# Kernel optimization log

Hardware: AMD Instinct MI355X
Metric: run time of the kernel (lower is better)

## Reference

```python
import jax, jax.numpy as jnp
import numpy as np

T = 2048        # tokens (flattened)
H = 2048        # hidden_size
NH = 16         # num_attention_heads
NKV = 4         # num_key_value_heads
HD = H // NH    # head_dim = 128
E = 8           # num_local_experts
TOPK = 2        # num_experts_per_tok
DFF = 4096      # expert intermediate size
EPS = 1e-5
THETA = 1000000.0


def setup_inputs() -> dict:
    key = jax.random.key(0)
    ks = jax.random.split(key, 10)
    s = 0.02
    return {
        "positions": jnp.arange(T, dtype=jnp.int32),
        "hidden_states": jax.random.normal(ks[0], (T, H), jnp.float32),
        "residual": jax.random.normal(ks[1], (T, H), jnp.float32),
        "ln1_w": jnp.ones((H,), jnp.float32),
        "ln2_w": jnp.ones((H,), jnp.float32),
        "wq": jax.random.normal(ks[2], (H, NH * HD), jnp.float32) * s,
        "wk": jax.random.normal(ks[3], (H, NKV * HD), jnp.float32) * s,
        "wv": jax.random.normal(ks[4], (H, NKV * HD), jnp.float32) * s,
        "wo": jax.random.normal(ks[5], (NH * HD, H), jnp.float32) * s,
        "gate_w": jax.random.normal(ks[6], (H, E), jnp.float32) * s,
        "w1": jax.random.normal(ks[7], (E, H, DFF), jnp.float32) * s,
        "w3": jax.random.normal(ks[8], (E, H, DFF), jnp.float32) * s,
        "w2": jax.random.normal(ks[9], (E, DFF, H), jnp.float32) * s,
    }


def _rmsnorm(x, w):
    v = jnp.mean(x * x, axis=-1, keepdims=True)
    return x * jax.lax.rsqrt(v + EPS) * w


def _rope(pos, x):
    # NeoX-style rotary; x: [T, nh, HD]
    half = HD // 2
    inv_freq = 1.0 / (THETA ** (jnp.arange(half, dtype=jnp.float32) / half))
    ang = pos.astype(jnp.float32)[:, None] * inv_freq          # [T, half]
    cos = jnp.cos(ang)[:, None, :]
    sin = jnp.sin(ang)[:, None, :]
    x1, x2 = jnp.split(x, 2, axis=-1)
    return jnp.concatenate([x1 * cos - x2 * sin, x2 * cos + x1 * sin], axis=-1)


def _forward(positions, hidden_states, residual, ln1_w, ln2_w,
             wq, wk, wv, wo, gate_w, w1, w3, w2):
    # fused add + RMSNorm (vLLM semantics)
    res = hidden_states + residual
    h = _rmsnorm(res, ln1_w)

    # attention with RoPE + GQA, causal
    q = (h @ wq).reshape(T, NH, HD)
    k = (h @ wk).reshape(T, NKV, HD)
    v = (h @ wv).reshape(T, NKV, HD)
    q = _rope(positions, q)
    k = _rope(positions, k)
    rep = NH // NKV
    k = jnp.repeat(k, rep, axis=1)   # [T, NH, HD]
    v = jnp.repeat(v, rep, axis=1)
    scores = jnp.einsum("thd,shd->hts", q, k) * (HD ** -0.5)   # [NH, T, T]
    causal = jnp.tril(jnp.ones((T, T), bool))
    scores = jnp.where(causal[None], scores, jnp.finfo(scores.dtype).min)
    p = jax.nn.softmax(scores, axis=-1)
    attn = jnp.einsum("hts,shd->thd", p, v).reshape(T, NH * HD) @ wo

    # fused add + RMSNorm
    res2 = attn + res
    h2 = _rmsnorm(res2, ln2_w)

    # MoE: softmax gate (fp32), top-k, renormalize, combine
    logits = h2 @ gate_w
    rw = jax.nn.softmax(logits.astype(jnp.float32), axis=-1)   # [T, E]
    w_top, idx = jax.lax.top_k(rw, TOPK)                        # [T, K]
    w_top = w_top / jnp.sum(w_top, axis=-1, keepdims=True)
    # per-token combine weight for each expert (sums duplicate selections)
    comb = jnp.zeros((T, E), jnp.float32).at[
        jnp.arange(T)[:, None], idx].add(w_top)                 # [T, E]

    out = jnp.zeros((T, H), h2.dtype)
    for e in range(E):  # small fixed expert count
        g = jax.nn.silu(h2 @ w1[e]) * (h2 @ w3[e])
        out = out + comb[:, e:e + 1] * (g @ w2[e])
    return out, res2


def reference(positions, hidden_states, residual, ln1_w, ln2_w,
              wq, wk, wv, wo, gate_w, w1, w3, w2):
    return _forward(positions, hidden_states, residual, ln1_w, ln2_w,
                    wq, wk, wv, wo, gate_w, w1, w3, w2)
```

## Files before the change

kernel.cpp:

```cpp
#include <hip/hip_runtime.h>
#include <math.h>

typedef unsigned short u16;
typedef __attribute__((ext_vector_type(8))) short bf16x8;
typedef __attribute__((ext_vector_type(4))) float f32x4;

#define DI __device__ __forceinline__

constexpr int Tt  = 2048;
constexpr int Hh  = 2048;
constexpr int DFFd = 4096;

DI u16 f2b(float f) {
  union { float f; unsigned u; } x; x.f = f;
  unsigned r = x.u + 0x7fffu + ((x.u >> 16) & 1u);
  return (u16)(r >> 16);
}
DI float b2f(u16 h) {
  union { unsigned u; float f; } x; x.u = ((unsigned)h) << 16; return x.f;
}
DI void gll16(const void* g, void* l) {
  __builtin_amdgcn_global_load_lds((const __attribute__((address_space(1))) unsigned int*)g,
                                   (__attribute__((address_space(3))) unsigned int*)l, 16, 0, 0);
}

__global__ void k_addnorm(const float* __restrict__ hs, const float* __restrict__ resid,
                          const float* __restrict__ w, float* __restrict__ resf,
                          u16* __restrict__ hb, u16* __restrict__ hblo) {
  const int t = blockIdx.x, tid = threadIdx.x, lane = tid & 63, wid = tid >> 6;
  __shared__ float red[4];
  const size_t base = (size_t)t * Hh;
  float4 a = *(const float4*)(hs + base + tid * 4);
  float4 b = *(const float4*)(resid + base + tid * 4);
  float4 c = *(const float4*)(hs + base + 1024 + tid * 4);
  float4 d = *(const float4*)(resid + base + 1024 + tid * 4);
  float4 r1 = {a.x + b.x, a.y + b.y, a.z + b.z, a.w + b.w};
  float4 r2 = {c.x + d.x, c.y + d.y, c.z + d.z, c.w + d.w};
  *(float4*)(resf + base + tid * 4) = r1;
  *(float4*)(resf + base + 1024 + tid * 4) = r2;
  float ss = r1.x*r1.x + r1.y*r1.y + r1.z*r1.z + r1.w*r1.w
           + r2.x*r2.x + r2.y*r2.y + r2.z*r2.z + r2.w*r2.w;
#pragma unroll
  for (int m = 1; m < 64; m <<= 1) ss += __shfl_xor(ss, m);
  if (lane == 0) red[wid] = ss;
  __syncthreads();
  float tot = red[0] + red[1] + red[2] + red[3];
  float rstd = rsqrtf(tot * (1.f / Hh) + 1e-5f);
  float4 w1v = *(const float4*)(w + tid * 4);
  float4 w2v = *(const float4*)(w + 1024 + tid * 4);
  float hv[8];
  hv[0] = r1.x * rstd * w1v.x; hv[1] = r1.y * rstd * w1v.y;
  hv[2] = r1.z * rstd * w1v.z; hv[3] = r1.w * rstd * w1v.w;
  hv[4] = r2.x * rstd * w2v.x; hv[5] = r2.y * rstd * w2v.y;
  hv[6] = r2.z * rstd * w2v.z; hv[7] = r2.w * rstd * w2v.w;
  ushort4 o1, o2, l1, l2;
  u16 h;
  h = f2b(hv[0]); o1.x = h; l1.x = f2b(hv[0] - b2f(h));
  h = f2b(hv[1]); o1.y = h; l1.y = f2b(hv[1] - b2f(h));
  h = f2b(hv[2]); o1.z = h; l1.z = f2b(hv[2] - b2f(h));
  h = f2b(hv[3]); o1.w = h; l1.w = f2b(hv[3] - b2f(h));
  h = f2b(hv[4]); o2.x = h; l2.x = f2b(hv[4] - b2f(h));
  h = f2b(hv[5]); o2.y = h; l2.y = f2b(hv[5] - b2f(h));
  h = f2b(hv[6]); o2.z = h; l2.z = f2b(hv[6] - b2f(h));
  h = f2b(hv[7]); o2.w = h; l2.w = f2b(hv[7] - b2f(h));
  *(ushort4*)(hb + base + tid * 4) = o1;
  *(ushort4*)(hb + base + 1024 + tid * 4) = o2;
  *(ushort4*)(hblo + base + tid * 4) = l1;
  *(ushort4*)(hblo + base + 1024 + tid * 4) = l2;
}

__global__ void k_transpose64(const float* __restrict__ src, u16* __restrict__ dst,
                              int K, int N) {
  size_t zo = (size_t)blockIdx.z * K * N;
  src += zo; dst += zo;
  __shared__ float tl[64][65];
  const int t = threadIdx.x;
  const int k0 = blockIdx.x * 64, n0 = blockIdx.y * 64;
  int r = t >> 4, c = (t & 15) * 4;
#pragma unroll
  for (int u = 0; u < 4; u++) {
    float4 v = *(const float4*)(src + (size_t)(k0 + r + u * 16) * N + n0 + c);
    tl[r + u * 16][c] = v.x; tl[r + u * 16][c + 1] = v.y;
    tl[r + u * 16][c + 2] = v.z; tl[r + u * 16][c + 3] = v.w;
  }
  __syncthreads();
  int n = t >> 2, kc = (t & 3) * 16;
  __align__(16) u16 tmp[16];
#pragma unroll
  for (int i = 0; i < 16; i++) tmp[i] = f2b(tl[kc + i][n]);
  uint4* dp = (uint4*)(dst + (size_t)(n0 + n) * K + k0 + kc);
  dp[0] = ((uint4*)tmp)[0];
  dp[1] = ((uint4*)tmp)[1];
}

__global__ void k_transpose2_64(const float* __restrict__ src, u16* __restrict__ dhi,
                                u16* __restrict__ dlo, int K, int N) {
  __shared__ float tl[64][65];
  const int t = threadIdx.x;
  const int k0 = blockIdx.x * 64, n0 = blockIdx.y * 64;
  int r = t >> 4, c = (t & 15) * 4;
#pragma unroll
  for (int u = 0; u < 4; u++) {
    float4 v = *(const float4*)(src + (size_t)(k0 + r + u * 16) * N + n0 + c);
    tl[r + u * 16][c] = v.x; tl[r + u * 16][c + 1] = v.y;
    tl[r + u * 16][c + 2] = v.z; tl[r + u * 16][c + 3] = v.w;
  }
  __syncthreads();
  int n = t >> 2, kc = (t & 3) * 16;
  __align__(16) u16 th[16], tlo[16];
#pragma unroll
  for (int i = 0; i < 16; i++) {
    float x = tl[kc + i][n];
    u16 hx = f2b(x);
    th[i] = hx; tlo[i] = f2b(x - b2f(hx));
  }
  uint4* dph = (uint4*)(dhi + (size_t)(n0 + n) * K + k0 + kc);
  dph[0] = ((uint4*)th)[0]; dph[1] = ((uint4*)th)[1];
  uint4* dpl = (uint4*)(dlo + (size_t)(n0 + n) * K + k0 + kc);
  dpl[0] = ((uint4*)tlo)[0]; dpl[1] = ((uint4*)tlo)[1];
}

__launch_bounds__(256, 2)
__global__ void gemm_qkv(const u16* __restrict__ Ahi, const u16* __restrict__ Alo,
                         const u16* __restrict__ Bhi, const u16* __restrict__ Blo,
                         float* __restrict__ C) {
  __shared__ __align__(16) u16 Ah[2][128 * 32];
  __shared__ __align__(16) u16 Al[2][128 * 32];
  __shared__ __align__(16) u16 Bh[2][128 * 32];
  __shared__ __align__(16) u16 Bl[2][128 * 32];
  const int tid = threadIdx.x;
  const int wid = tid >> 6, lane = tid & 63, lr = lane & 15, lg = lane >> 4;
  const int m0 = blockIdx.x * 128, n0 = blockIdx.y * 128;
  const int wm = (wid >> 1) * 64, wn = (wid & 1) * 64;
  const int c0 = tid, c1 = tid + 256;
  const int ss0 = ((c0 & 3) ^ ((c0 >> 3) & 3)) * 8;
  const int ss1 = ((c1 & 3) ^ ((c1 >> 3) & 3)) * 8;
  const int fs = (lg ^ ((lr >> 1) & 3)) * 8;
  const size_t ao0 = (size_t)(m0 + (c0 >> 2)) * 2048 + ss0;
  const size_t ao1 = (size_t)(m0 + (c1 >> 2)) * 2048 + ss1;
  const size_t bo0 = (size_t)(n0 + (c0 >> 2)) * 2048 + ss0;
  const size_t bo1 = (size_t)(n0 + (c1 >> 2)) * 2048 + ss1;
  f32x4 zv = {0.f, 0.f, 0.f, 0.f};
  f32x4 acc[4][4];
#pragma unroll
  for (int i = 0; i < 4; i++)
#pragma unroll
    for (int j = 0; j < 4; j++) acc[i][j] = zv;
  const int NT = 2048 >> 5;
  gll16(Ahi + ao0, &Ah[0][c0 * 8]); gll16(Ahi + ao1, &Ah[0][c1 * 8]);
  gll16(Alo + ao0, &Al[0][c0 * 8]); gll16(Alo + ao1, &Al[0][c1 * 8]);
  gll16(Bhi + bo0, &Bh[0][c0 * 8]); gll16(Bhi + bo1, &Bh[0][c1 * 8]);
  gll16(Blo + bo0, &Bl[0][c0 * 8]); gll16(Blo + bo1, &Bl[0][c1 * 8]);
  int cur = 0;
  for (int t = 0; t < NT; ++t) {
    __syncthreads();
    if (t + 1 < NT) {
      int ko = (t + 1) << 5;
      gll16(Ahi + ao0 + ko, &Ah[cur ^ 1][c0 * 8]); gll16(Ahi + ao1 + ko, &Ah[cur ^ 1][c1 * 8]);
      gll16(Alo + ao0 + ko, &Al[cur ^ 1][c0 * 8]); gll16(Alo + ao1 + ko, &Al[cur ^ 1][c1 * 8]);
      gll16(Bhi + bo0 + ko, &Bh[cur ^ 1][c0 * 8]); gll16(Bhi + bo1 + ko, &Bh[cur ^ 1][c1 * 8]);
      gll16(Blo + bo0 + ko, &Bl[cur ^ 1][c0 * 8]); gll16(Blo + bo1 + ko, &Bl[cur ^ 1][c1 * 8]);
    }
    bf16x8 ah[4], al[4], bh[4], bl[4];
#pragma unroll
    for (int i = 0; i < 4; i++) {
      ah[i] = *(const bf16x8*)&Ah[cur][(wm + i * 16 + lr) * 32 + fs];
      al[i] = *(const bf16x8*)&Al[cur][(wm + i * 16 + lr) * 32 + fs];
    }
#pragma unroll
    for (int j = 0; j < 4; j++) {
      bh[j] = *(const bf16x8*)&Bh[cur][(wn + j * 16 + lr) * 32 + fs];
      bl[j] = *(const bf16x8*)&Bl[cur][(wn + j * 16 + lr) * 32 + fs];
    }
#pragma unroll
    for (int i = 0; i < 4; i++)
#pragma unroll
      for (int j = 0; j < 4; j++) {
        acc[i][j] = __builtin_amdgcn_mfma_f32_16x16x32_bf16(ah[i], bh[j], acc[i][j], 0, 0, 0);
        acc[i][j] = __builtin_amdgcn_mfma_f32_16x16x32_bf16(ah[i], bl[j], acc[i][j], 0, 0, 0);
        acc[i][j] = __builtin_amdgcn_mfma_f32_16x16x32_bf16(al[i], bh[j], acc[i][j], 0, 0, 0);
      }
    cur ^= 1;
  }
#pragma unroll
  for (int i = 0; i < 4; i++) {
    const int row = m0 + wm + i * 16 + lg * 4;
#pragma unroll
    for (int j = 0; j < 4; j++) {
      const int col = n0 + wn + j * 16 + lr;
#pragma unroll
      for (int r = 0; r < 4; r++)
        C[(size_t)(row + r) * 3072 + col] = acc[i][j][r];
    }
  }
}

template <int MODE>
__launch_bounds__(256, 4)
__global__ void gemm_bt(const u16* __restrict__ A, const u16* __restrict__ BT,
                        float* __restrict__ C, const float* __restrict__ addf,
                        int N, int K) {
  __shared__ __align__(16) u16 Albuf[2][128 * 32];
  __shared__ __align__(16) u16 Blbuf[2][128 * 32];
  const int tid = threadIdx.x;
  const int wid = tid >> 6, lane = tid & 63, lr = lane & 15, lg = lane >> 4;
  const int m0 = blockIdx.x * 128, n0 = blockIdx.y * 128;
  const int wm = (wid >> 1) * 64, wn = (wid & 1) * 64;
  const int c0 = tid, c1 = tid + 256;
  const int ss0 = ((c0 & 3) ^ ((c0 >> 3) & 3)) * 8;
  const int ss1 = ((c1 & 3) ^ ((c1 >> 3) & 3)) * 8;
  const int fs = (lg ^ ((lr >> 1) & 3)) * 8;
  const u16* a0 = A + (size_t)(m0 + (c0 >> 2)) * K + ss0;
  const u16* a1 = A + (size_t)(m0 + (c1 >> 2)) * K + ss1;
  const u16* b0 = BT + (size_t)(n0 + (c0 >> 2)) * K + ss0;
  const u16* b1 = BT + (size_t)(n0 + (c1 >> 2)) * K + ss1;
  f32x4 zv = {0.f, 0.f, 0.f, 0.f};
  f32x4 acc[4][4];
#pragma unroll
  for (int i = 0; i < 4; i++)
#pragma unroll
    for (int j = 0; j < 4; j++) acc[i][j] = zv;
  const int NT = K >> 5;
  gll16(a0, &Albuf[0][c0 * 8]); gll16(a1, &Albuf[0][c1 * 8]);
  gll16(b0, &Blbuf[0][c0 * 8]); gll16(b1, &Blbuf[0][c1 * 8]);
  int cur = 0;
  for (int t = 0; t < NT; ++t) {
    __syncthreads();
    if (t + 1 < NT) {
      int ko = (t + 1) << 5;
      gll16(a0 + ko, &Albuf[cur ^ 1][c0 * 8]); gll16(a1 + ko, &Albuf[cur ^ 1][c1 * 8]);
      gll16(b0 + ko, &Blbuf[cur ^ 1][c0 * 8]); gll16(b1 + ko, &Blbuf[cur ^ 1][c1 * 8]);
    }
    bf16x8 af[4], bf[4];
#pragma unroll
    for (int i = 0; i < 4; i++) af[i] = *(const bf16x8*)&Albuf[cur][(wm + i * 16 + lr) * 32 + fs];
#pragma unroll
    for (int j = 0; j < 4; j++) bf[j] = *(const bf16x8*)&Blbuf[cur][(wn + j * 16 + lr) * 32 + fs];
#pragma unroll
    for (int i = 0; i < 4; i++)
#pragma unroll
      for (int j = 0; j < 4; j++)
        acc[i][j] = __builtin_amdgcn_mfma_f32_16x16x32_bf16(af[i], bf[j], acc[i][j], 0, 0, 0);
    cur ^= 1;
  }
#pragma unroll
  for (int i = 0; i < 4; i++) {
    const int row = m0 + wm + i * 16 + lg * 4;
#pragma unroll
    for (int j = 0; j < 4; j++) {
      const int col = n0 + wn + j * 16 + lr;
#pragma unroll
      for (int r = 0; r < 4; r++) {
        float v = acc[i][j][r];
        if (MODE == 1) v += addf[(size_t)(row + r) * N + col];
        C[(size_t)(row + r) * N + col] = v;
      }
    }
  }
}

__global__ void k_rope(const int* __restrict__ pos, const float* __restrict__ qkvf,
                       u16* __restrict__ qhi, u16* __restrict__ qlo,
                       u16* __restrict__ khi, u16* __restrict__ klo,
                       u16* __restrict__ vb) {
  __shared__ float invtab[64];
  const int t = blockIdx.x, tid = threadIdx.x;
  if (tid < 64) invtab[tid] = 1.0f / (float)pow(1.0e6, (double)tid / 64.0);
  __syncthreads();
  const float p = (float)pos[t];
  const float* src = qkvf + (size_t)t * 3072;
#pragma unroll
  for (int it = 0; it < 4; ++it) {
    int idx = tid + it * 256;
    int head = idx >> 6, i = idx & 63;
    float ang = p * invtab[i];
    float cc, ssn;
    sincosf(ang, &ssn, &cc);
    float x1 = src[head * 128 + i], x2 = src[head * 128 + i + 64];
    float y1 = x1 * cc - x2 * ssn;
    float y2 = x2 * cc + x1 * ssn;
    u16 h1 = f2b(y1), h2 = f2b(y2);
    size_t o1 = (size_t)t * 2048 + head * 128 + i;
    qhi[o1] = h1;      qlo[o1] = f2b(y1 - b2f(h1));
    qhi[o1 + 64] = h2; qlo[o1 + 64] = f2b(y2 - b2f(h2));
  }
  {
    int head = tid >> 6, i = tid & 63;
    float ang = p * invtab[i];
    float cc, ssn;
    sincosf(ang, &ssn, &cc);
    float x1 = src[2048 + head * 128 + i], x2 = src[2048 + head * 128 + i + 64];
    float y1 = x1 * cc - x2 * ssn;
    float y2 = x2 * cc + x1 * ssn;
    u16 h1 = f2b(y1), h2 = f2b(y2);
    size_t o1 = (size_t)t * 512 + head * 128 + i;
    khi[o1] = h1;      klo[o1] = f2b(y1 - b2f(h1));
    khi[o1 + 64] = h2; klo[o1 + 64] = f2b(y2 - b2f(h2));
  }
#pragma unroll
  for (int u = 0; u < 2; ++u) {
    int ccol = tid + u * 256;
    vb[(size_t)t * 512 + ccol] = f2b(src[2560 + ccol]);
  }
}

__global__ void k_G(const float* __restrict__ ln2w, const float* __restrict__ gw,
                    float* __restrict__ G) {
  int i = blockIdx.x * 256 + threadIdx.x;
  G[i] = ln2w[i >> 3] * gw[i];
}
__global__ void k_WG(const float* __restrict__ wo, const float* __restrict__ G,
                     float* __restrict__ WG) {
  int i = blockIdx.x * 256 + threadIdx.x;
  int r = i >> 3, e = i & 7;
  const float* wr_ = wo + (size_t)r * 2048;
  float s0 = 0, s1 = 0, s2 = 0, s3 = 0;
  for (int c = 0; c < 2048; c += 4) {
    s0 += wr_[c] * G[c * 8 + e];
    s1 += wr_[c + 1] * G[(c + 1) * 8 + e];
    s2 += wr_[c + 2] * G[(c + 2) * 8 + e];
    s3 += wr_[c + 3] * G[(c + 3) * 8 + e];
  }
  WG[i] = (s0 + s1) + (s2 + s3);
}
__global__ void k_resG(const float* __restrict__ resf, const float* __restrict__ G,
                       float* __restrict__ resG) {
  int i = blockIdx.x * 256 + threadIdx.x;
  int t = i >> 3, e = i & 7;
  const float* rr = resf + (size_t)t * 2048;
  float s0 = 0, s1 = 0, s2 = 0, s3 = 0;
  for (int c = 0; c < 2048; c += 4) {
    s0 += rr[c] * G[c * 8 + e];
    s1 += rr[c + 1] * G[(c + 1) * 8 + e];
    s2 += rr[c + 2] * G[(c + 2) * 8 + e];
    s3 += rr[c + 3] * G[(c + 3) * 8 + e];
  }
  resG[i] = (s0 + s1) + (s2 + s3);
}
__global__ void k_VG(const float* __restrict__ qkvf, const float* __restrict__ WG,
                     float* __restrict__ VG) {
  int i = blockIdx.x * 256 + threadIdx.x;
  int e = i & 7, t = (i >> 3) & 2047, h = i >> 14;
  const float* vr = qkvf + (size_t)t * 3072 + 2560 + (h >> 2) * 128;
  const float* wgr = WG + (size_t)(h * 128) * 8 + e;
  float s = 0;
#pragma unroll 4
  for (int d = 0; d < 128; d++) s += vr[d] * wgr[d * 8];
  VG[i] = s;
}

__launch_bounds__(256, 2)
__global__ void k_attn2(const u16* __restrict__ qh, const u16* __restrict__ qlo,
                        const u16* __restrict__ kh, const u16* __restrict__ klo,
                        const u16* __restrict__ vb, const float* __restrict__ vg,
                        u16* __restrict__ attnb, float* __restrict__ pvgp) {
  __shared__ __align__(16) u16 Kh[64 * 128];
  __shared__ __align__(16) u16 Kl[64 * 128];
  __shared__ __align__(16) u16 VTl[128 * 64];
  __shared__ __align__(16) u16 Pl[4][16 * 72];
  const int tid = threadIdx.x, wid = tid >> 6, lane = tid & 63, lr = lane & 15, lg = lane >> 4;
  const int h = blockIdx.y, hk = h >> 2, wr = wid * 16;
  f32x4 zv = {0.f, 0.f, 0.f, 0.f};

  for (int half = 0; half < 2; ++half) {
    const int qt = half ? blockIdx.x : 31 - blockIdx.x;
    const int q0 = qt * 64;
    float m_[4], l_[4], avg[4][8];
    f32x4 accO[8];
#pragma unroll
    for (int r = 0; r < 4; r++) {
      m_[r] = -3e38f; l_[r] = 0.f;
#pragma unroll
      for (int e = 0; e < 8; e++) avg[r][e] = 0.f;
    }
#pragma unroll
    for (int d = 0; d < 8; d++) accO[d] = zv;
    bf16x8 aqh[4], aql[4];
    {
      const size_t qb = (size_t)(q0 + wr + lr) * 2048 + h * 128 + lg * 8;
#pragma unroll
      for (int kk = 0; kk < 4; kk++) {
        aqh[kk] = *(const bf16x8*)(qh + qb + kk * 32);
        aql[kk] = *(const bf16x8*)(qlo + qb + kk * 32);
      }
    }
    const int nk = qt + 1;
    for (int kt = 0; kt < nk; ++kt) {
      const int s0 = kt * 64;
      __syncthreads();
#pragma unroll
      for (int i = 0; i < 4; i++) {
        int c = tid + i * 256;
        int s = c >> 4, b = (c & 15) * 8;
        size_t go = (size_t)(s0 + s) * 512 + hk * 128 + (b ^ ((s & 7) << 3));
        gll16(kh + go, &Kh[c * 8]);
        gll16(klo + go, &Kl[c * 8]);
      }
      {
        int s = tid >> 2;
        const u16* vsrc = vb + (size_t)(s0 + s) * 512 + hk * 128 + (tid & 3) * 32;
#pragma unroll
        for (int u = 0; u < 4; u++) {
          uint4 wv = *(const uint4*)(vsrc + u * 8);
          const u16* tp = (const u16*)&wv;
          int d0b = (tid & 3) * 32 + u * 8;
          int scol = s ^ (((d0b >> 3) & 7) << 3);
#pragma unroll
          for (int ii = 0; ii < 8; ii++) VTl[(d0b + ii) * 64 + scol] = tp[ii];
        }
      }
      float vgr[4][8];
#pragma unroll
      for (int ct = 0; ct < 4; ct++) {
        const float* vp = vg + ((size_t)h * 2048 + s0 + ct * 16 + lr) * 8;
        float4 u0 = *(const float4*)vp;
        float4 u1 = *(const float4*)(vp + 4);
        vgr[ct][0] = u0.x; vgr[ct][1] = u0.y; vgr[ct][2] = u0.z; vgr[ct][3] = u0.w;
        vgr[ct][4] = u1.x; vgr[ct][5] = u1.y; vgr[ct][6] = u1.z; vgr[ct][7] = u1.w;
      }
      __syncthreads();
      f32x4 accS[4];
#pragma unroll
      for (int ct = 0; ct < 4; ct++) accS[ct] = zv;
      __builtin_amdgcn_s_setprio(1);
#pragma unroll
      for (int kk = 0; kk < 4; kk++) {
#pragma unroll
        for (int ct = 0; ct < 4; ct++) {
          int off = (ct * 16 + lr) * 128 + ((kk * 32 + lg * 8) ^ ((lr & 7) << 3));
          bf16x8 bh = *(const bf16x8*)&Kh[off];
          bf16x8 bl = *(const bf16x8*)&Kl[off];
          accS[ct] = __builtin_amdgcn_mfma_f32_16x16x32_bf16(aqh[kk], bh, accS[ct], 0, 0, 0);
          accS[ct] = __builtin_amdgcn_mfma_f32_16x16x32_bf16(aqh[kk], bl, accS[ct], 0, 0, 0);
          accS[ct] = __builtin_amdgcn_mfma_f32_16x16x32_bf16(aql[kk], bh, accS[ct], 0, 0, 0);
        }
      }
      __builtin_amdgcn_s_setprio(0);
      const bool diag = (kt == qt);
      float alpha[4];
#pragma unroll
      for (int r = 0; r < 4; r++) {
        float sv[4];
        float mx = -3e38f;
#pragma unroll
        for (int ct = 0; ct < 4; ct++) {
          float sc = accS[ct][r] * 0.08838834764831845f;
          if (diag) {
            int col = ct * 16 + lr;
            int row = wr + lg * 4 + r;
            if (col > row) sc = -3e38f;
          }
          sv[ct] = sc; mx = fmaxf(mx, sc);
        }
#pragma unroll
        for (int m2 = 1; m2 < 16; m2 <<= 1) mx = fmaxf(mx, __shfl_xor(mx, m2));
        float mnew = fmaxf(m_[r], mx);
        float a = expf(m_[r] - mnew);
        float pv[4];
        float rs = 0.f;
#pragma unroll
        for (int ct = 0; ct < 4; ct++) { pv[ct] = expf(sv[ct] - mnew); rs += pv[ct]; }
#pragma unroll
        for (int m2 = 1; m2 < 16; m2 <<= 1) rs += __shfl_xor(rs, m2);
        l_[r] = l_[r] * a + rs;
        m_[r] = mnew;
        alpha[r] = a;
#pragma unroll
        for (int e = 0; e < 8; e++) avg[r][e] *= a;
#pragma unroll
        for (int ct = 0; ct < 4; ct++) {
          Pl[wid][(lg * 4 + r) * 72 + ct * 16 + lr] = f2b(pv[ct]);
#pragma unroll
          for (int e = 0; e < 8; e++) avg[r][e] += pv[ct] * vgr[ct][e];
        }
      }
#pragma unroll
      for (int d = 0; d < 8; d++)
#pragma unroll
        for (int r = 0; r < 4; r++) accO[d][r] *= alpha[r];
      __builtin_amdgcn_s_setprio(1);
#pragma unroll
      for (int ks = 0; ks < 2; ks++) {
        bf16x8 ap = *(const bf16x8*)&Pl[wid][lr * 72 + ks * 32 + lg * 8];
#pragma unroll
        for (int d0 = 0; d0 < 8; d0++) {
          int d = d0 * 16 + lr;
          int scol = (ks * 32 + lg * 8) ^ (((d >> 3) & 7) << 3);
          bf16x8 bv = *(const bf16x8*)&VTl[d * 64 + scol];
          accO[d0] = __builtin_amdgcn_mfma_f32_16x16x32_bf16(ap, bv, accO[d0], 0, 0, 0);
        }
      }
      __builtin_amdgcn_s_setprio(0);
    }
#pragma unroll
    for (int d0 = 0; d0 < 8; d0++)
#pragma unroll
      for (int r = 0; r < 4; r++) {
        float v = accO[d0][r] / l_[r];
        attnb[(size_t)(q0 + wr + lg * 4 + r) * 2048 + h * 128 + d0 * 16 + lr] = f2b(v);
      }
#pragma unroll
    for (int m2 = 1; m2 < 16; m2 <<= 1)
#pragma unroll
      for (int r = 0; r < 4; r++)
#pragma unroll
        for (int e = 0; e < 8; e++) avg[r][e] += __shfl_xor(avg[r][e], m2);
#pragma unroll
    for (int r = 0; r < 4; r++) {
      int t = q0 + wr + lg * 4 + r;
      float inv = 1.f / l_[r];
#pragma unroll
      for (int e = 0; e < 8; e++)
        if (lr == e) pvgp[((size_t)h * 2048 + t) * 8 + e] = avg[r][e] * inv;
    }
  }
}

__global__ void k_ln2gate(const float* __restrict__ res2, const float* __restrict__ w,
                          const float* __restrict__ resG, const float* __restrict__ pvgp,
                          u16* __restrict__ h2b,
                          int* __restrict__ cnt, int* __restrict__ tok,
                          float* __restrict__ wgt, int* __restrict__ jid) {
  const int t = blockIdx.x, tid = threadIdx.x, lane = tid & 63, wid = tid >> 6;
  __shared__ float red[4];
  const size_t base = (size_t)t * Hh;
  float4 r1 = *(const float4*)(res2 + base + tid * 4);
  float4 r2 = *(const float4*)(res2 + base + 1024 + tid * 4);
  float ss = r1.x*r1.x + r1.y*r1.y + r1.z*r1.z + r1.w*r1.w
           + r2.x*r2.x + r2.y*r2.y + r2.z*r2.z + r2.w*r2.w;
#pragma unroll
  for (int m = 1; m < 64; m <<= 1) ss += __shfl_xor(ss, m);
  if (lane == 0) red[wid] = ss;
  __syncthreads();
  float tot = red[0] + red[1] + red[2] + red[3];
  float rstd = rsqrtf(tot * (1.f / Hh) + 1e-5f);
  float4 w1v = *(const float4*)(w + tid * 4);
  float4 w2v = *(const float4*)(w + 1024 + tid * 4);
  ushort4 o1, o2;
  o1.x = f2b(r1.x * rstd * w1v.x); o1.y = f2b(r1.y * rstd * w1v.y);
  o1.z = f2b(r1.z * rstd * w1v.z); o1.w = f2b(r1.w * rstd * w1v.w);
  o2.x = f2b(r2.x * rstd * w2v.x); o2.y = f2b(r2.y * rstd * w2v.y);
  o2.z = f2b(r2.z * rstd * w2v.z); o2.w = f2b(r2.w * rstd * w2v.w);
  *(ushort4*)(h2b + base + tid * 4) = o1;
  *(ushort4*)(h2b + base + 1024 + tid * 4) = o2;
  if (tid == 0) {
    float lg8[8];
#pragma unroll
    for (int e = 0; e < 8; e++) {
      float s = resG[t * 8 + e];
      for (int hh = 0; hh < 16; hh++) s += pvgp[((size_t)hh * 2048 + t) * 8 + e];
      lg8[e] = s * rstd;
    }
    float mx = lg8[0];
#pragma unroll
    for (int e = 1; e < 8; e++) mx = fmaxf(mx, lg8[e]);
    float ex[8];
#pragma unroll
    for (int e = 0; e < 8; e++) ex[e] = expf(lg8[e] - mx);
    int i1 = 0; float v1 = ex[0];
#pragma unroll
    for (int e = 1; e < 8; e++) if (ex[e] > v1) { v1 = ex[e]; i1 = e; }
    int i2 = -1; float v2 = -1.f;
#pragma unroll
    for (int e = 0; e < 8; e++) if (e != i1 && ex[e] > v2) { v2 = ex[e]; i2 = e; }
    float inv = 1.f / (v1 + v2);
    int s1 = atomicAdd(&cnt[i1], 1);
    tok[i1 * 2048 + s1] = t; wgt[i1 * 2048 + s1] = v1 * inv; jid[i1 * 2048 + s1] = 0;
    int s2 = atomicAdd(&cnt[i2], 1);
    tok[i2 * 2048 + s2] = t; wgt[i2 * 2048 + s2] = v2 * inv; jid[i2 * 2048 + s2] = 1;
  }
}

template <int PHASE>
__launch_bounds__(256, 4)
__global__ void gemm_m13(const u16* __restrict__ h2b, const u16* __restrict__ wT,
                         u16* __restrict__ gbuf, float* __restrict__ x1,
                         const int* __restrict__ cnt, const int* __restrict__ tok) {
  const int e = blockIdx.z;
  const int cnt_e = cnt[e];
  const int m0 = blockIdx.y * 128;
  if (m0 >= cnt_e) return;
  int gb = 0;
#pragma unroll
  for (int i = 0; i < 8; i++) if (i < e) gb += cnt[i];
  __shared__ __align__(16) u16 Al[2][128 * 32];
  __shared__ __align__(16) u16 Bl[2][128 * 32];
  const int tid = threadIdx.x;
  const int wid = tid >> 6, lane = tid & 63, lr = lane & 15, lg = lane >> 4;
  const int n0 = blockIdx.x * 128;
  const int wm = (wid >> 1) * 64, wn = (wid & 1) * 64;
  const int c0 = tid, c1 = tid + 256;
  const int ss0 = ((c0 & 3) ^ ((c0 >> 3) & 3)) * 8;
  const int ss1 = ((c1 & 3) ^ ((c1 >> 3) & 3)) * 8;
  const int fs = (lg ^ ((lr >> 1) & 3)) * 8;
  int r0 = m0 + (c0 >> 2); if (r0 > cnt_e - 1) r0 = cnt_e - 1;
  int r1 = m0 + (c1 >> 2); if (r1 > cnt_e - 1) r1 = cnt_e - 1;
  const int tk0 = tok[e * 2048 + r0], tk1 = tok[e * 2048 + r1];
  const u16* a0 = h2b + (size_t)tk0 * 2048 + ss0;
  const u16* a1 = h2b + (size_t)tk1 * 2048 + ss1;
  const u16* b0 = wT + (size_t)e * DFFd * 2048 + (size_t)(n0 + (c0 >> 2)) * 2048 + ss0;
  const u16* b1 = wT + (size_t)e * DFFd * 2048 + (size_t)(n0 + (c1 >> 2)) * 2048 + ss1;
  f32x4 zv = {0.f, 0.f, 0.f, 0.f};
  f32x4 acc[4][4];
#pragma unroll
  for (int i = 0; i < 4; i++)
#pragma unroll
    for (int j = 0; j < 4; j++) acc[i][j] = zv;
  const int NT = 2048 >> 5;
  gll16(a0, &Al[0][c0 * 8]); gll16(a1, &Al[0][c1 * 8]);
  gll16(b0, &Bl[0][c0 * 8]); gll16(b1, &Bl[0][c1 * 8]);
  int cur = 0;
  for (int t = 0; t < NT; ++t) {
    __syncthreads();
    if (t + 1 < NT) {
      int ko = (t + 1) << 5;
      gll16(a0 + ko, &Al[cur ^ 1][c0 * 8]); gll16(a1 + ko, &Al[cur ^ 1][c1 * 8]);
      gll16(b0 + ko, &Bl[cur ^ 1][c0 * 8]); gll16(b1 + ko, &Bl[cur ^ 1][c1 * 8]);
    }
    bf16x8 af[4], bf[4];
#pragma unroll
    for (int i = 0; i < 4; i++) af[i] = *(const bf16x8*)&Al[cur][(wm + i * 16 + lr) * 32 + fs];
#pragma unroll
    for (int j = 0; j < 4; j++) bf[j] = *(const bf16x8*)&Bl[cur][(wn + j * 16 + lr) * 32 + fs];
#pragma unroll
    for (int i = 0; i < 4; i++)
#pragma unroll
      for (int j = 0; j < 4; j++)
        acc[i][j] = __builtin_amdgcn_mfma_f32_16x16x32_bf16(af[i], bf[j], acc[i][j], 0, 0, 0);
    cur ^= 1;
  }
#pragma unroll
  for (int i = 0; i < 4; i++) {
    const int slotb = m0 + wm + i * 16 + lg * 4;
#pragma unroll
    for (int j = 0; j < 4; j++) {
      const int col = n0 + wn + j * 16 + lr;
#pragma unroll
      for (int r = 0; r < 4; r++) {
        int slot = slotb + r;
        if (slot < cnt_e) {
          size_t o = (size_t)(gb + slot) * DFFd + col;
          if (PHASE == 0) {
            x1[o] = acc[i][j][r];
          } else {
            float xv = x1[o];
            float g = xv / (1.f + __expf(-xv)) * acc[i][j][r];
            gbuf[o] = f2b(g);
          }
        }
      }
    }
  }
}

__launch_bounds__(256, 4)
__global__ void gemm2k(const u16* __restrict__ gbuf, const u16* __restrict__ w2T,
                       float* __restrict__ outk, const int* __restrict__ cnt,
                       const int* __restrict__ tok, const float* __restrict__ wgt,
                       const int* __restrict__ jid) {
  const int e = blockIdx.z;
  const int cnt_e = cnt[e];
  const int m0 = blockIdx.y * 128;
  if (m0 >= cnt_e) return;
  int gb = 0;
#pragma unroll
  for (int i = 0; i < 8; i++) if (i < e) gb += cnt[i];
  __shared__ __align__(16) u16 Al[2][128 * 32];
  __shared__ __align__(16) u16 Bl[2][128 * 32];
  const int tid = threadIdx.x;
  const int wid = tid >> 6, lane = tid & 63, lr = lane & 15, lg = lane >> 4;
  const int n0 = blockIdx.x * 128;
  const int wm = (wid >> 1) * 64, wn = (wid & 1) * 64;
  const int c0 = tid, c1 = tid + 256;
  const int ss0 = ((c0 & 3) ^ ((c0 >> 3) & 3)) * 8;
  const int ss1 = ((c1 & 3) ^ ((c1 >> 3) & 3)) * 8;
  const int fs = (lg ^ ((lr >> 1) & 3)) * 8;
  const u16* A = gbuf + (size_t)gb * DFFd;
  const u16* a0 = A + (size_t)(m0 + (c0 >> 2)) * DFFd + ss0;
  const u16* a1 = A + (size_t)(m0 + (c1 >> 2)) * DFFd + ss1;
  const u16* b0 = w2T + (size_t)e * 2048 * DFFd + (size_t)(n0 + (c0 >> 2)) * DFFd + ss0;
  const u16* b1 = w2T + (size_t)e * 2048 * DFFd + (size_t)(n0 + (c1 >> 2)) * DFFd + ss1;
  f32x4 zv = {0.f, 0.f, 0.f, 0.f};
  f32x4 acc[4][4];
#pragma unroll
  for (int i = 0; i < 4; i++)
#pragma unroll
    for (int j = 0; j < 4; j++) acc[i][j] = zv;
  const int NT = DFFd >> 5;
  gll16(a0, &Al[0][c0 * 8]); gll16(a1, &Al[0][c1 * 8]);
  gll16(b0, &Bl[0][c0 * 8]); gll16(b1, &Bl[0][c1 * 8]);
  int cur = 0;
  for (int t = 0; t < NT; ++t) {
    __syncthreads();
    if (t + 1 < NT) {
      int ko = (t + 1) << 5;
      gll16(a0 + ko, &Al[cur ^ 1][c0 * 8]); gll16(a1 + ko, &Al[cur ^ 1][c1 * 8]);
      gll16(b0 + ko, &Bl[cur ^ 1][c0 * 8]); gll16(b1 + ko, &Bl[cur ^ 1][c1 * 8]);
    }
    bf16x8 af[4], bf[4];
#pragma unroll
    for (int i = 0; i < 4; i++) af[i] = *(const bf16x8*)&Al[cur][(wm + i * 16 + lr) * 32 + fs];
#pragma unroll
    for (int j = 0; j < 4; j++) bf[j] = *(const bf16x8*)&Bl[cur][(wn + j * 16 + lr) * 32 + fs];
#pragma unroll
    for (int i = 0; i < 4; i++)
#pragma unroll
      for (int j = 0; j < 4; j++)
        acc[i][j] = __builtin_amdgcn_mfma_f32_16x16x32_bf16(af[i], bf[j], acc[i][j], 0, 0, 0);
    cur ^= 1;
  }
#pragma unroll
  for (int i = 0; i < 4; i++) {
    const int slotb = m0 + wm + i * 16 + lg * 4;
#pragma unroll
    for (int r = 0; r < 4; r++) {
      int slot = slotb + r;
      if (slot < cnt_e) {
        int tkn = tok[e * 2048 + slot];
        float wv = wgt[e * 2048 + slot];
        int jj = jid[e * 2048 + slot];
        float* orow = outk + (size_t)jj * ((size_t)Tt * Hh) + (size_t)tkn * Hh;
#pragma unroll
        for (int j = 0; j < 4; j++) {
          const int col = n0 + wn + j * 16 + lr;
          orow[col] = wv * acc[i][j][r];
        }
      }
    }
  }
}

__global__ void k_zero(int* cnt) { if (threadIdx.x < 8) cnt[threadIdx.x] = 0; }

__global__ void k_combine(const float* __restrict__ outk, float* __restrict__ dout) {
  size_t i = ((size_t)blockIdx.x * 256 + threadIdx.x) * 4;
  float4 a = *(const float4*)(outk + i);
  float4 b = *(const float4*)(outk + (size_t)Tt * Hh + i);
  float4 o = {a.x + b.x, a.y + b.y, a.z + b.z, a.w + b.w};
  *(float4*)(dout + i) = o;
}

extern "C" void kernel_launch(void* const* d_in, const int* in_sizes, int n_in,
                              void* d_out, int out_size, void* d_ws, size_t ws_size,
                              hipStream_t stream) {
  const int*   positions = (const int*)d_in[0];
  const float* hs    = (const float*)d_in[1];
  const float* resid = (const float*)d_in[2];
  const float* ln1w  = (const float*)d_in[3];
  const float* ln2w  = (const float*)d_in[4];
  const float* wq    = (const float*)d_in[5];
  const float* wk    = (const float*)d_in[6];
  const float* wv    = (const float*)d_in[7];
  const float* wo    = (const float*)d_in[8];
  const float* gatew = (const float*)d_in[9];
  const float* w1    = (const float*)d_in[10];
  const float* w3    = (const float*)d_in[11];
  const float* w2    = (const float*)d_in[12];
  float* dout = (float*)d_out;
  float* res2 = dout + (size_t)Tt * Hh;

  char* wp = (char*)d_ws;
  auto take = [&](size_t bytes) -> void* {
    void* p = (void*)wp;
    wp += (bytes + 255) & ~(size_t)255;
    return p;
  };
  u16*   qkvT  = (u16*)  take((size_t)3072 * 2048 * 2);
  u16*   qkvTl = (u16*)  take((size_t)3072 * 2048 * 2);
  u16*   woT   = (u16*)  take((size_t)2048 * 2048 * 2);
  u16*   w1T   = (u16*)  take((size_t)8 * 4096 * 2048 * 2);
  u16*   w3T   = (u16*)  take((size_t)8 * 4096 * 2048 * 2);
  u16*   w2T   = (u16*)  take((size_t)8 * 2048 * 4096 * 2);
  float* resf  = (float*)take((size_t)Tt * Hh * 4);
  u16*   hb    = (u16*)  take((size_t)Tt * Hh * 2);
  u16*   hblo  = (u16*)  take((size_t)Tt * Hh * 2);
  float* qkvf  = (float*)take((size_t)Tt * 3072 * 4);
  u16*   qhi   = (u16*)  take((size_t)Tt * 2048 * 2);
  u16*   qlo   = (u16*)  take((size_t)Tt * 2048 * 2);
  u16*   khi   = (u16*)  take((size_t)Tt * 512 * 2);
  u16*   klo   = (u16*)  take((size_t)Tt * 512 * 2);
  u16*   vb2   = (u16*)  take((size_t)Tt * 512 * 2);
  u16*   attnb = (u16*)  take((size_t)Tt * 2048 * 2);
  u16*   h2b   = (u16*)  take((size_t)Tt * Hh * 2);
  u16*   gbuf  = (u16*)  take((size_t)(4096 + 128) * 4096 * 2);
  float* outk  = (float*)take((size_t)2 * Tt * Hh * 4);
  float* Gb    = (float*)take((size_t)2048 * 8 * 4);
  float* WGb   = (float*)take((size_t)2048 * 8 * 4);
  float* resGb = (float*)take((size_t)Tt * 8 * 4);
  float* VGb   = (float*)take((size_t)16 * Tt * 8 * 4);
  float* pvgp  = (float*)take((size_t)16 * Tt * 8 * 4);
  int*   tok   = (int*)  take((size_t)8 * 2048 * 4);
  float* wgt   = (float*)take((size_t)8 * 2048 * 4);
  int*   jid   = (int*)  take((size_t)8 * 2048 * 4);
  int*   cnt   = (int*)  take(64);
  if ((size_t)(wp - (char*)d_ws) > ws_size) return;
  float* x1buf = resf;

  k_zero<<<1, 64, 0, stream>>>(cnt);
  k_addnorm<<<Tt, 256, 0, stream>>>(hs, resid, ln1w, resf, hb, hblo);
  k_transpose2_64<<<dim3(32, 32, 1), 256, 0, stream>>>(wq, qkvT, qkvTl, 2048, 2048);
  k_transpose2_64<<<dim3(32, 8, 1), 256, 0, stream>>>(wk, qkvT + (size_t)2048 * 2048,
                                                      qkvTl + (size_t)2048 * 2048, 2048, 512);
  k_transpose2_64<<<dim3(32, 8, 1), 256, 0, stream>>>(wv, qkvT + (size_t)2560 * 2048,
                                                      qkvTl + (size_t)2560 * 2048, 2048, 512);
  k_transpose64<<<dim3(32, 32, 1), 256, 0, stream>>>(wo, woT, 2048, 2048);
  k_transpose64<<<dim3(32, 64, 8), 256, 0, stream>>>(w1, w1T, 2048, 4096);
  k_transpose64<<<dim3(32, 64, 8), 256, 0, stream>>>(w3, w3T, 2048, 4096);
  k_transpose64<<<dim3(64, 32, 8), 256, 0, stream>>>(w2, w2T, 4096, 2048);
  k_G<<<64, 256, 0, stream>>>(ln2w, gatew, Gb);
  k_WG<<<64, 256, 0, stream>>>(wo, Gb, WGb);
  k_resG<<<64, 256, 0, stream>>>(resf, Gb, resGb);
  gemm_qkv<<<dim3(16, 24, 1), 256, 0, stream>>>(hb, hblo, qkvT, qkvTl, qkvf);
  k_rope<<<Tt, 256, 0, stream>>>(positions, qkvf, qhi, qlo, khi, klo, vb2);
  k_VG<<<1024, 256, 0, stream>>>(qkvf, WGb, VGb);
  k_attn2<<<dim3(16, 16, 1), 256, 0, stream>>>(qhi, qlo, khi, klo, vb2, VGb, attnb, pvgp);
  gemm_bt<1><<<dim3(16, 16, 1), 256, 0, stream>>>(attnb, woT, res2, resf, 2048, 2048);
  k_ln2gate<<<Tt, 256, 0, stream>>>(res2, ln2w, resGb, pvgp, h2b, cnt, tok, wgt, jid);
  gemm_m13<0><<<dim3(32, 16, 8), 256, 0, stream>>>(h2b, w1T, gbuf, x1buf, cnt, tok);
  gemm_m13<1><<<dim3(32, 16, 8), 256, 0, stream>>>(h2b, w3T, gbuf, x1buf, cnt, tok);
  gemm2k<<<dim3(16, 16, 8), 256, 0, stream>>>(gbuf, w2T, outk, cnt, tok, wgt, jid);
  k_combine<<<4096, 256, 0, stream>>>(outk, dout);
}
```

Baseline: 1.235 ms.

## Fuse w1/w3 expert GEMMs with SiLU and split-K the w2 GEMM

Merges the two gate/up expert GEMM passes into one kernel that computes both w1 and w3 accumulators on a shared A tile and applies SiLU*mul in the epilogue. This removes the fp32 x1 intermediate round-trip and a second gather of the A rows. The down-projection GEMM is split into two K halves written to separate output buffers, which doubles the grid for better CU fill, and the combine kernel now sums four partial buffers. The cost is extra output traffic, and the fused kernel uses narrower N tiles (64) with more accumulator registers.

```diff
diff --git a/kernel.cpp b/kernel.cpp
--- a/kernel.cpp
+++ b/kernel.cpp
@@ -571,14 +571,99 @@
   }
 }
 
-template <int PHASE>
 __launch_bounds__(256, 4)
-__global__ void gemm_m13(const u16* __restrict__ h2b, const u16* __restrict__ wT,
-                         u16* __restrict__ gbuf, float* __restrict__ x1,
-                         const int* __restrict__ cnt, const int* __restrict__ tok) {
+__global__ void gemm13f(const u16* __restrict__ h2b, const u16* __restrict__ w1T,
+                        const u16* __restrict__ w3T, u16* __restrict__ gbuf,
+                        const int* __restrict__ cnt, const int* __restrict__ tok) {
   const int e = blockIdx.z;
   const int cnt_e = cnt[e];
   const int m0 = blockIdx.y * 128;
+  if (m0 >= cnt_e) return;
+  int gb = 0;
+#pragma unroll
+  for (int i = 0; i < 8; i++) if (i < e) gb += cnt[i];
+  __shared__ __align__(16) u16 Al[2][128 * 32];
+  __shared__ __align__(16) u16 B1l[2][64 * 32];
+  __shared__ __align__(16) u16 B3l[2][64 * 32];
+  const int tid = threadIdx.x;
+  const int wid = tid >> 6, lane = tid & 63, lr = lane & 15, lg = lane >> 4;
+  const int n0 = blockIdx.x * 64;
+  const int wm = (wid >> 1) * 64, wn = (wid & 1) * 32;
+  const int c0 = tid, c1 = tid + 256;
+  const int ss0 = ((c0 & 3) ^ ((c0 >> 3) & 3)) * 8;
+  const int ss1 = ((c1 & 3) ^ ((c1 >> 3) & 3)) * 8;
+  const int fs = (lg ^ ((lr >> 1) & 3)) * 8;
+  int r0 = m0 + (c0 >> 2); if (r0 > cnt_e - 1) r0 = cnt_e - 1;
+  int r1 = m0 + (c1 >> 2); if (r1 > cnt_e - 1) r1 = cnt_e - 1;
+  const int tk0 = tok[e * 2048 + r0], tk1 = tok[e * 2048 + r1];
+  const u16* a0 = h2b + (size_t)tk0 * 2048 + ss0;
+  const u16* a1 = h2b + (size_t)tk1 * 2048 + ss1;
+  const size_t wbase = (size_t)e * DFFd * 2048 + (size_t)(n0 + (c0 >> 2)) * 2048 + ss0;
+  const u16* b1p = w1T + wbase;
+  const u16* b3p = w3T + wbase;
+  f32x4 zv = {0.f, 0.f, 0.f, 0.f};
+  f32x4 acc1[4][2], acc3[4][2];
+#pragma unroll
+  for (int i = 0; i < 4; i++)
+#pragma unroll
+    for (int j = 0; j < 2; j++) { acc1[i][j] = zv; acc3[i][j] = zv; }
+  const int NT = 2048 >> 5;
+  gll16(a0, &Al[0][c0 * 8]); gll16(a1, &Al[0][c1 * 8]);
+  gll16(b1p, &B1l[0][c0 * 8]); gll16(b3p, &B3l[0][c0 * 8]);
+  int cur = 0;
+  for (int t = 0; t < NT; ++t) {
+    __syncthreads();
+    if (t + 1 < NT) {
+      int ko = (t + 1) << 5;
+      gll16(a0 + ko, &Al[cur ^ 1][c0 * 8]); gll16(a1 + ko, &Al[cur ^ 1][c1 * 8]);
+      gll16(b1p + ko, &B1l[cur ^ 1][c0 * 8]); gll16(b3p + ko, &B3l[cur ^ 1][c0 * 8]);
+    }
+    bf16x8 af[4], b1f[2], b3f[2];
+#pragma unroll
+    for (int i = 0; i < 4; i++) af[i] = *(const bf16x8*)&Al[cur][(wm + i * 16 + lr) * 32 + fs];
+#pragma unroll
+    for (int j = 0; j < 2; j++) {
+      b1f[j] = *(const bf16x8*)&B1l[cur][(wn + j * 16 + lr) * 32 + fs];
+      b3f[j] = *(const bf16x8*)&B3l[cur][(wn + j * 16 + lr) * 32 + fs];
+    }
+#pragma unroll
+    for (int i = 0; i < 4; i++)
+#pragma unroll
+      for (int j = 0; j < 2; j++) {
+        acc1[i][j] = __builtin_amdgcn_mfma_f32_16x16x32_bf16(af[i], b1f[j], acc1[i][j], 0, 0, 0);
+        acc3[i][j] = __builtin_amdgcn_mfma_f32_16x16x32_bf16(af[i], b3f[j], acc3[i][j], 0, 0, 0);
+      }
+    cur ^= 1;
+  }
+#pragma unroll
+  for (int i = 0; i < 4; i++) {
+    const int slotb = m0 + wm + i * 16 + lg * 4;
+#pragma unroll
+    for (int j = 0; j < 2; j++) {
+      const int col = n0 + wn + j * 16 + lr;
+#pragma unroll
+      for (int r = 0; r < 4; r++) {
+        int slot = slotb + r;
+        if (slot < cnt_e) {
+          float xv = acc1[i][j][r];
+          float g = xv / (1.f + __expf(-xv)) * acc3[i][j][r];
+          gbuf[(size_t)(gb + slot) * DFFd + col] = f2b(g);
+        }
+      }
+    }
+  }
+}
+
+__launch_bounds__(256, 4)
+__global__ void gemm2k(const u16* __restrict__ gbuf, const u16* __restrict__ w2T,
+                       float* __restrict__ outk, float* __restrict__ outkx,
+                       const int* __restrict__ cnt,
+                       const int* __restrict__ tok, const float* __restrict__ wgt,
+                       const int* __restrict__ jid) {
+  const int e = blockIdx.z;
+  const int cnt_e = cnt[e];
+  const int kh = blockIdx.y & 1;
+  const int m0 = (blockIdx.y >> 1) * 128;
   if (m0 >= cnt_e) return;
   int gb = 0;
 #pragma unroll
@@ -593,13 +678,12 @@
   const int ss0 = ((c0 & 3) ^ ((c0 >> 3) & 3)) * 8;
   const int ss1 = ((c1 & 3) ^ ((c1 >> 3) & 3)) * 8;
   const int fs = (lg ^ ((lr >> 1) & 3)) * 8;
-  int r0 = m0 + (c0 >> 2); if (r0 > cnt_e - 1) r0 = cnt_e - 1;
-  int r1 = m0 + (c1 >> 2); if (r1 > cnt_e - 1) r1 = cnt_e - 1;
-  const int tk0 = tok[e * 2048 + r0], tk1 = tok[e * 2048 + r1];
-  const u16* a0 = h2b + (size_t)tk0 * 2048 + ss0;
-  const u16* a1 = h2b + (size_t)tk1 * 2048 + ss1;
-  const u16* b0 = wT + (size_t)e * DFFd * 2048 + (size_t)(n0 + (c0 >> 2)) * 2048 + ss0;
-  const u16* b1 = wT + (size_t)e * DFFd * 2048 + (size_t)(n0 + (c1 >> 2)) * 2048 + ss1;
+  const int k0 = kh * 2048;
+  const u16* A = gbuf + (size_t)gb * DFFd + k0;
+  const u16* a0 = A + (size_t)(m0 + (c0 >> 2)) * DFFd + ss0;
+  const u16* a1 = A + (size_t)(m0 + (c1 >> 2)) * DFFd + ss1;
+  const u16* b0 = w2T + (size_t)e * 2048 * DFFd + (size_t)(n0 + (c0 >> 2)) * DFFd + k0 + ss0;
+  const u16* b1 = w2T + (size_t)e * 2048 * DFFd + (size_t)(n0 + (c1 >> 2)) * DFFd + k0 + ss1;
   f32x4 zv = {0.f, 0.f, 0.f, 0.f};
   f32x4 acc[4][4];
 #pragma unroll
@@ -629,86 +713,7 @@
         acc[i][j] = __builtin_amdgcn_mfma_f32_16x16x32_bf16(af[i], bf[j], acc[i][j], 0, 0, 0);
     cur ^= 1;
   }
-#pragma unroll
-  for (int i = 0; i < 4; i++) {
-    const int slotb = m0 + wm + i * 16 + lg * 4;
-#pragma unroll
-    for (int j = 0; j < 4; j++) {
-      const int col = n0 + wn + j * 16 + lr;
-#pragma unroll
-      for (int r = 0; r < 4; r++) {
-        int slot = slotb + r;
-        if (slot < cnt_e) {
-          size_t o = (size_t)(gb + slot) * DFFd + col;
-          if (PHASE == 0) {
-            x1[o] = acc[i][j][r];
-          } else {
-            float xv = x1[o];
-            float g = xv / (1.f + __expf(-xv)) * acc[i][j][r];
-            gbuf[o] = f2b(g);
-          }
-        }
-      }
-    }
-  }
-}
-
-__launch_bounds__(256, 4)
-__global__ void gemm2k(const u16* __restrict__ gbuf, const u16* __restrict__ w2T,
-                       float* __restrict__ outk, const int* __restrict__ cnt,
-                       const int* __restrict__ tok, const float* __restrict__ wgt,
-                       const int* __restrict__ jid) {
-  const int e = blockIdx.z;
-  const int cnt_e = cnt[e];
-  const int m0 = blockIdx.y * 128;
-  if (m0 >= cnt_e) return;
-  int gb = 0;
-#pragma unroll
-  for (int i = 0; i < 8; i++) if (i < e) gb += cnt[i];
-  __shared__ __align__(16) u16 Al[2][128 * 32];
-  __shared__ __align__(16) u16 Bl[2][128 * 32];
-  const int tid = threadIdx.x;
-  const int wid = tid >> 6, lane = tid & 63, lr = lane & 15, lg = lane >> 4;
-  const int n0 = blockIdx.x * 128;
-  const int wm = (wid >> 1) * 64, wn = (wid & 1) * 64;
-  const int c0 = tid, c1 = tid + 256;
-  const int ss0 = ((c0 & 3) ^ ((c0 >> 3) & 3)) * 8;
-  const int ss1 = ((c1 & 3) ^ ((c1 >> 3) & 3)) * 8;
-  const int fs = (lg ^ ((lr >> 1) & 3)) * 8;
-  const u16* A = gbuf + (size_t)gb * DFFd;
-  const u16* a0 = A + (size_t)(m0 + (c0 >> 2)) * DFFd + ss0;
-  const u16* a1 = A + (size_t)(m0 + (c1 >> 2)) * DFFd + ss1;
-  const u16* b0 = w2T + (size_t)e * 2048 * DFFd + (size_t)(n0 + (c0 >> 2)) * DFFd + ss0;
-  const u16* b1 = w2T + (size_t)e * 2048 * DFFd + (size_t)(n0 + (c1 >> 2)) * DFFd + ss1;
-  f32x4 zv = {0.f, 0.f, 0.f, 0.f};
-  f32x4 acc[4][4];
-#pragma unroll
-  for (int i = 0; i < 4; i++)
-#pragma unroll
-    for (int j = 0; j < 4; j++) acc[i][j] = zv;
-  const int NT = DFFd >> 5;
-  gll16(a0, &Al[0][c0 * 8]); gll16(a1, &Al[0][c1 * 8]);
-  gll16(b0, &Bl[0][c0 * 8]); gll16(b1, &Bl[0][c1 * 8]);
-  int cur = 0;
-  for (int t = 0; t < NT; ++t) {
-    __syncthreads();
-    if (t + 1 < NT) {
-      int ko = (t + 1) << 5;
-      gll16(a0 + ko, &Al[cur ^ 1][c0 * 8]); gll16(a1 + ko, &Al[cur ^ 1][c1 * 8]);
-      gll16(b0 + ko, &Bl[cur ^ 1][c0 * 8]); gll16(b1 + ko, &Bl[cur ^ 1][c1 * 8]);
-    }
-    bf16x8 af[4], bf[4];
-#pragma unroll
-    for (int i = 0; i < 4; i++) af[i] = *(const bf16x8*)&Al[cur][(wm + i * 16 + lr) * 32 + fs];
-#pragma unroll
-    for (int j = 0; j < 4; j++) bf[j] = *(const bf16x8*)&Bl[cur][(wn + j * 16 + lr) * 32 + fs];
-#pragma unroll
-    for (int i = 0; i < 4; i++)
-#pragma unroll
-      for (int j = 0; j < 4; j++)
-        acc[i][j] = __builtin_amdgcn_mfma_f32_16x16x32_bf16(af[i], bf[j], acc[i][j], 0, 0, 0);
-    cur ^= 1;
-  }
+  float* basep = kh ? outkx : outk;
 #pragma unroll
   for (int i = 0; i < 4; i++) {
     const int slotb = m0 + wm + i * 16 + lg * 4;
@@ -719,7 +724,7 @@
         int tkn = tok[e * 2048 + slot];
         float wv = wgt[e * 2048 + slot];
         int jj = jid[e * 2048 + slot];
-        float* orow = outk + (size_t)jj * ((size_t)Tt * Hh) + (size_t)tkn * Hh;
+        float* orow = basep + (size_t)jj * ((size_t)Tt * Hh) + (size_t)tkn * Hh;
 #pragma unroll
         for (int j = 0; j < 4; j++) {
           const int col = n0 + wn + j * 16 + lr;
@@ -732,11 +737,15 @@
 
 __global__ void k_zero(int* cnt) { if (threadIdx.x < 8) cnt[threadIdx.x] = 0; }
 
-__global__ void k_combine(const float* __restrict__ outk, float* __restrict__ dout) {
+__global__ void k_combine(const float* __restrict__ outk, const float* __restrict__ outkx,
+                          float* __restrict__ dout) {
   size_t i = ((size_t)blockIdx.x * 256 + threadIdx.x) * 4;
   float4 a = *(const float4*)(outk + i);
   float4 b = *(const float4*)(outk + (size_t)Tt * Hh + i);
-  float4 o = {a.x + b.x, a.y + b.y, a.z + b.z, a.w + b.w};
+  float4 c = *(const float4*)(outkx + i);
+  float4 d = *(const float4*)(outkx + (size_t)Tt * Hh + i);
+  float4 o = {a.x + b.x + c.x + d.x, a.y + b.y + c.y + d.y,
+              a.z + b.z + c.z + d.z, a.w + b.w + c.w + d.w};
   *(float4*)(dout + i) = o;
 }
 
@@ -794,7 +803,7 @@
   int*   jid   = (int*)  take((size_t)8 * 2048 * 4);
   int*   cnt   = (int*)  take(64);
   if ((size_t)(wp - (char*)d_ws) > ws_size) return;
-  float* x1buf = resf;
+  float* outkx = resf;
 
   k_zero<<<1, 64, 0, stream>>>(cnt);
   k_addnorm<<<Tt, 256, 0, stream>>>(hs, resid, ln1w, resf, hb, hblo);
@@ -816,8 +825,7 @@
   k_attn2<<<dim3(16, 16, 1), 256, 0, stream>>>(qhi, qlo, khi, klo, vb2, VGb, attnb, pvgp);
   gemm_bt<1><<<dim3(16, 16, 1), 256, 0, stream>>>(attnb, woT, res2, resf, 2048, 2048);
   k_ln2gate<<<Tt, 256, 0, stream>>>(res2, ln2w, resGb, pvgp, h2b, cnt, tok, wgt, jid);
-  gemm_m13<0><<<dim3(32, 16, 8), 256, 0, stream>>>(h2b, w1T, gbuf, x1buf, cnt, tok);
-  gemm_m13<1><<<dim3(32, 16, 8), 256, 0, stream>>>(h2b, w3T, gbuf, x1buf, cnt, tok);
-  gemm2k<<<dim3(16, 16, 8), 256, 0, stream>>>(gbuf, w2T, outk, cnt, tok, wgt, jid);
-  k_combine<<<4096, 256, 0, stream>>>(outk, dout);
-}
+  gemm13f<<<dim3(64, 16, 8), 256, 0, stream>>>(h2b, w1T, w3T, gbuf, cnt, tok);
+  gemm2k<<<dim3(16, 32, 8), 256, 0, stream>>>(gbuf, w2T, outk, outkx, cnt, tok, wgt, jid);
+  k_combine<<<4096, 256, 0, stream>>>(outk, outkx, dout);
+}
```

After: 1.148 ms (median of 3 runs). 1.08x faster.
